# Performance work log

Hardware: AMD Instinct MI355X
Metric: run time of the kernel (lower is better)

## Reference

```python
import jax, jax.numpy as jnp
import numpy as np

H = 16
D_MODEL = 1024
D_K = D_MODEL // H
B, S = 4, 2048


def setup_inputs() -> dict:
    key = jax.random.key(0)
    ks = jax.random.split(key, 12)
    scale = 1.0 / np.sqrt(D_MODEL)
    inp = {
        "query": jax.random.normal(ks[0], (B, S, D_MODEL), jnp.float32),
        "key_in": jax.random.normal(ks[1], (B, S, D_MODEL), jnp.float32),
        "value": jax.random.normal(ks[2], (B, S, D_MODEL), jnp.float32),
        "mask": jax.random.randint(ks[3], (B, 1, S, S), 0, 2, jnp.int32),
    }
    # 4 Linear(d_model, d_model) layers: Wq, Wk, Wv, Wo (+ biases)
    names = ["q", "k", "v", "o"]
    for i, n in enumerate(names):
        inp[f"W{n}"] = jax.random.normal(ks[4 + i], (D_MODEL, D_MODEL), jnp.float32) * scale
        inp[f"b{n}"] = jax.random.normal(ks[8 + i], (D_MODEL,), jnp.float32) * scale
    return inp


def reference(query, key_in, value, mask, Wq, bq, Wk, bk, Wv, bv, Wo, bo):
    # Linear projections then split heads: [B,S,D] -> [B,H,S,Dk]
    def proj(x, W, b):
        y = jnp.einsum("bsd,ed->bse", x, W) + b  # torch Linear: x @ W.T + b
        return y.reshape(B, S, H, D_K).transpose(0, 2, 1, 3)

    q = proj(query, Wq, bq)
    k = proj(key_in, Wk, bk)
    v = proj(value, Wv, bv)

    scores = jnp.einsum("bhqd,bhkd->bhqk", q, k) / jnp.sqrt(jnp.float32(D_K))
    scores = jnp.where(mask == 0, jnp.float32(-1e9), scores)
    p_attn = jax.nn.softmax(scores, axis=-1)
    # dropout is identity in eval mode
    x = jnp.einsum("bhqk,bhkd->bhqd", p_attn, v)
    x = x.transpose(0, 2, 1, 3).reshape(B, S, D_MODEL)
    return jnp.einsum("bsd,ed->bse", x, Wo) + bo
```

## Files before the change

### kernel.cpp

```cpp
#include <hip/hip_runtime.h>
#include <hip/hip_bf16.h>

typedef __bf16 bf16_t;
typedef __attribute__((ext_vector_type(8))) __bf16 bf16x8;
typedef __attribute__((ext_vector_type(4))) __bf16 bf16x4;
typedef __attribute__((ext_vector_type(4))) float f32x4;
typedef __attribute__((ext_vector_type(16))) float f32x16;

#define GAS __attribute__((address_space(1)))
#define LAS __attribute__((address_space(3)))

__device__ __forceinline__ void async_copy16(const bf16_t* g, bf16_t* l) {
    __builtin_amdgcn_global_load_lds((const GAS void*)g, (LAS void*)l, 16, 0, 0);
}

__global__ __launch_bounds__(256) void convert_kernel(
    const float* __restrict__ src, bf16_t* __restrict__ dst, int n)
{
    int i = (blockIdx.x * 256 + threadIdx.x) * 8;
    if (i >= n) return;
    f32x4 f0 = *(const f32x4*)(src + i);
    f32x4 f1 = *(const f32x4*)(src + i + 4);
    bf16x8 v;
#pragma unroll
    for (int j = 0; j < 4; j++) { v[j] = (bf16_t)f0[j]; v[4 + j] = (bf16_t)f1[j]; }
    *(bf16x8*)&dst[i] = v;
}

__global__ __launch_bounds__(256) void pack_mask_kernel(
    const int* __restrict__ mask, unsigned long long* __restrict__ out)
{
    int i = blockIdx.x * 256 + threadIdx.x;
    unsigned long long bits = __ballot(mask[i] != 0);
    if ((threadIdx.x & 63) == 0) out[i >> 6] = bits;
}

template<int MODE>
__global__ __launch_bounds__(256, 2) void gemm_nt(
    const bf16_t* __restrict__ A, const bf16_t* __restrict__ W,
    const float* __restrict__ bias, void* __restrict__ out_, float oscale)
{
    __shared__ __align__(16) bf16_t Als[128 * 32];
    __shared__ __align__(16) bf16_t Bls[128 * 32];

    const int tid  = threadIdx.x;
    const int wave = tid >> 6, lane = tid & 63;
    const int quad = lane >> 4, lq = lane & 15;
    const int wm = wave >> 1, wn = wave & 1;
    const int tm = blockIdx.x * 128, tn = blockIdx.y * 128;
    const int K = 1024;

    const bf16_t* gA0 = A + (size_t)(tm + wave * 32 + (lane >> 2)) * K + (lane & 3) * 8;
    const bf16_t* gA1 = gA0 + (size_t)16 * K;
    const bf16_t* gB0 = W + (size_t)(tn + wave * 32 + (lane >> 2)) * K + (lane & 3) * 8;
    const bf16_t* gB1 = gB0 + (size_t)16 * K;
    bf16_t* lA0 = &Als[(wave * 32) * 32];
    bf16_t* lA1 = &Als[(wave * 32 + 16) * 32];
    bf16_t* lB0 = &Bls[(wave * 32) * 32];
    bf16_t* lB1 = &Bls[(wave * 32 + 16) * 32];

    f32x4 acc[4][4] = {};

    for (int k0 = 0; k0 < K; k0 += 32) {
        __syncthreads();
        async_copy16(gA0, lA0);
        async_copy16(gA1, lA1);
        async_copy16(gB0, lB0);
        async_copy16(gB1, lB1);
        gA0 += 32; gA1 += 32; gB0 += 32; gB1 += 32;
        __syncthreads();

        bf16x8 af[4], bfr[4];
#pragma unroll
        for (int i = 0; i < 4; i++) {
            af[i]  = *(const bf16x8*)&Als[(wm * 64 + i * 16 + lq) * 32 + quad * 8];
            bfr[i] = *(const bf16x8*)&Bls[(wn * 64 + i * 16 + lq) * 32 + quad * 8];
        }
#pragma unroll
        for (int i = 0; i < 4; i++)
#pragma unroll
            for (int j = 0; j < 4; j++) {
                if (MODE == 2)
                    acc[i][j] = __builtin_amdgcn_mfma_f32_16x16x32_bf16(bfr[j], af[i], acc[i][j], 0, 0, 0);
                else
                    acc[i][j] = __builtin_amdgcn_mfma_f32_16x16x32_bf16(af[i], bfr[j], acc[i][j], 0, 0, 0);
            }
    }

    float* outf = (float*)out_;
    bf16_t* outb = (bf16_t*)out_;
#pragma unroll
    for (int i = 0; i < 4; i++)
#pragma unroll
        for (int j = 0; j < 4; j++)
#pragma unroll
            for (int r = 0; r < 4; r++) {
                float v = acc[i][j][r];
                if (MODE == 0) {
                    int row = tm + wm * 64 + i * 16 + quad * 4 + r;
                    int col = tn + wn * 64 + j * 16 + lq;
                    outf[(size_t)row * 1024 + col] = (v + bias[col]) * oscale;
                } else if (MODE == 1) {
                    int row = tm + wm * 64 + i * 16 + quad * 4 + r;
                    int col = tn + wn * 64 + j * 16 + lq;
                    v = (v + bias[col]) * oscale;
                    int b = row >> 11, s = row & 2047;
                    int h = col >> 6,  dk = col & 63;
                    outb[(((size_t)(b * 16 + h) * 2048 + s) << 6) + dk] = (bf16_t)v;
                } else {
                    int n = tn + wn * 64 + j * 16 + quad * 4 + r;
                    int m = tm + wm * 64 + i * 16 + lq;
                    v = (v + bias[n]) * oscale;
                    int b = m >> 11, s = m & 2047;
                    int h = n >> 6,  dk = n & 63;
                    outb[((size_t)((b * 16 + h) * 64 + dk) << 11) + s] = (bf16_t)v;
                }
            }
}

#define LDP 68

__global__ __launch_bounds__(64, 2) void attn_kernel(
    const bf16_t* __restrict__ Q, const bf16_t* __restrict__ Kh,
    const bf16_t* __restrict__ Vt, const unsigned int* __restrict__ mp,
    bf16_t* __restrict__ X)
{
    __shared__ __align__(16) bf16_t Pls[64 * LDP];

    const int lane = threadIdx.x;
    const int l31  = lane & 31;
    const int hi8  = (lane >> 5) * 8, hi4 = (lane >> 5) * 4;
    const int bh = blockIdx.y;
    const int b  = bh >> 4, h = bh & 15;
    const int qb = blockIdx.x * 64;

    bf16x8 qf[2][4];
#pragma unroll
    for (int qg = 0; qg < 2; qg++) {
        const bf16_t* qp = Q + ((size_t)bh * 2048 + qb + qg * 32 + l31) * 64 + hi8;
#pragma unroll
        for (int c = 0; c < 4; c++) qf[qg][c] = *(const bf16x8*)(qp + c * 16);
    }

    f32x16 od[2][2] = {};
    float lsum[2] = {0.f, 0.f};

    const bf16_t* kbase = Kh + ((size_t)bh * 2048 + l31) * 64 + hi8;
    const bf16_t* vb0   = Vt + ((size_t)bh * 64 + l31) * 2048 + hi8;
    const bf16_t* vb1   = vb0 + (size_t)32 * 2048;

    const unsigned long long* mq0 =
        (const unsigned long long*)mp + ((size_t)(b << 11) + qb + l31) * 32;
    const unsigned long long* mq1 = mq0 + 32 * 32;

    bf16_t* pw = &Pls[0];

    for (int kt = 0; kt < 32; kt++) {
        unsigned long long mw[2] = { mq0[kt], mq1[kt] };
        const bf16_t* kk = kbase + (size_t)(kt * 64) * 64;

#pragma unroll
        for (int kh = 0; kh < 2; kh++) {
            bf16x8 kf[4];
            const bf16_t* krow = kk + (size_t)(kh * 32) * 64;
#pragma unroll
            for (int c = 0; c < 4; c++)
                kf[c] = *(const bf16x8*)(krow + c * 16);

#pragma unroll
            for (int qg = 0; qg < 2; qg++) {
                f32x16 z = {};
                z = __builtin_amdgcn_mfma_f32_32x32x16_bf16(kf[0], qf[qg][0], z, 0, 0, 0);
                z = __builtin_amdgcn_mfma_f32_32x32x16_bf16(kf[1], qf[qg][1], z, 0, 0, 0);
                z = __builtin_amdgcn_mfma_f32_32x32x16_bf16(kf[2], qf[qg][2], z, 0, 0, 0);
                z = __builtin_amdgcn_mfma_f32_32x32x16_bf16(kf[3], qf[qg][3], z, 0, 0, 0);
                unsigned int mbits = (unsigned int)(mw[qg] >> (kh * 32 + hi4));
                float ls = 0.f;
#pragma unroll
                for (int p = 0; p < 4; p++) {
                    bf16x4 pk;
#pragma unroll
                    for (int r = 0; r < 4; r++) {
                        float sv = ((mbits >> (8 * p + r)) & 1) ? z[4 * p + r] : -1e9f;
                        float e = __expf(sv);
                        ls += e;
                        pk[r] = (bf16_t)e;
                    }
                    *(bf16x4*)&pw[(qg * 32 + l31) * LDP + kh * 32 + 8 * p + hi4] = pk;
                }
                lsum[qg] += ls;
            }
        }

#pragma unroll
        for (int kh = 0; kh < 2; kh++) {
            bf16x8 pf[2][2];
#pragma unroll
            for (int qg = 0; qg < 2; qg++) {
                const bf16_t* prow = &pw[(qg * 32 + l31) * LDP + kh * 32 + hi8];
                pf[qg][0] = *(const bf16x8*)(prow);
                pf[qg][1] = *(const bf16x8*)(prow + 16);
            }
            const size_t voff = (size_t)(kt * 64 + kh * 32);
#pragma unroll
            for (int c = 0; c < 2; c++) {
                bf16x8 vf0 = *(const bf16x8*)(vb0 + voff + c * 16);
                bf16x8 vf1 = *(const bf16x8*)(vb1 + voff + c * 16);
                od[0][0] = __builtin_amdgcn_mfma_f32_32x32x16_bf16(vf0, pf[0][c], od[0][0], 0, 0, 0);
                od[1][0] = __builtin_amdgcn_mfma_f32_32x32x16_bf16(vf0, pf[1][c], od[1][0], 0, 0, 0);
                od[0][1] = __builtin_amdgcn_mfma_f32_32x32x16_bf16(vf1, pf[0][c], od[0][1], 0, 0, 0);
                od[1][1] = __builtin_amdgcn_mfma_f32_32x32x16_bf16(vf1, pf[1][c], od[1][1], 0, 0, 0);
            }
        }
    }

#pragma unroll
    for (int qg = 0; qg < 2; qg++) {
        float l = lsum[qg] + __shfl_xor(lsum[qg], 32);
        float rl = (l > 0.f) ? 1.0f / l : 0.f;
        int qrow = qb + qg * 32 + l31;
        bf16_t* xp = X + ((size_t)(b * 2048) + qrow) * 1024 + h * 64 + hi4;
#pragma unroll
        for (int dt = 0; dt < 2; dt++)
#pragma unroll
            for (int p = 0; p < 4; p++) {
                bf16x4 ov;
#pragma unroll
                for (int r = 0; r < 4; r++)
                    ov[r] = (bf16_t)(od[qg][dt][p * 4 + r] * rl);
                *(bf16x4*)(xp + dt * 32 + p * 8) = ov;
            }
    }
}

extern "C" void kernel_launch(void* const* d_in, const int* in_sizes, int n_in,
                              void* d_out, int out_size, void* d_ws, size_t ws_size,
                              hipStream_t stream)
{
    const float* query  = (const float*)d_in[0];
    const float* key_in = (const float*)d_in[1];
    const float* value  = (const float*)d_in[2];
    const int*   mask   = (const int*)d_in[3];

    char* ws = (char*)d_ws;
    const size_t SZ  = (size_t)8192 * 1024 * 2;
    const size_t MPK = (size_t)2 * 1024 * 1024;
    const size_t WSZ = (size_t)1024 * 1024 * 2;
    bf16_t* C   = (bf16_t*)(ws);
    bf16_t* Qb  = (bf16_t*)(ws + SZ);
    bf16_t* Kb  = (bf16_t*)(ws + 2 * SZ);
    bf16_t* Vtb = (bf16_t*)(ws + 3 * SZ);
    unsigned long long* mpack = (unsigned long long*)(ws + 4 * SZ);
    bf16_t* Wc[4];
    for (int i = 0; i < 4; i++)
        Wc[i] = (bf16_t*)(ws + 4 * SZ + MPK + i * WSZ);

    const size_t NEED = 4 * SZ + MPK + 4 * WSZ;
    if (ws_size < NEED) return;

    const int NACT = 8192 * 1024;
    for (int i = 0; i < 4; i++)
        convert_kernel<<<512, 256, 0, stream>>>((const float*)d_in[4 + 2 * i],
                                                Wc[i], 1024 * 1024);
    pack_mask_kernel<<<65536, 256, 0, stream>>>(mask, mpack);

    dim3 gg(64, 8);
    convert_kernel<<<4096, 256, 0, stream>>>(query, C, NACT);
    gemm_nt<1><<<gg, 256, 0, stream>>>(C, Wc[0], (const float*)d_in[5], Qb, 0.125f);
    convert_kernel<<<4096, 256, 0, stream>>>(key_in, C, NACT);
    gemm_nt<1><<<gg, 256, 0, stream>>>(C, Wc[1], (const float*)d_in[7], Kb, 1.0f);
    convert_kernel<<<4096, 256, 0, stream>>>(value, C, NACT);
    gemm_nt<2><<<gg, 256, 0, stream>>>(C, Wc[2], (const float*)d_in[9], Vtb, 1.0f);

    attn_kernel<<<dim3(32, 64), 64, 0, stream>>>(Qb, Kb, Vtb,
                                                 (const unsigned int*)mpack, C);
    gemm_nt<0><<<gg, 256, 0, stream>>>(C, Wc[3], (const float*)d_in[11], d_out, 1.0f);
}
```

Before: 486.6 us.

## Split attention key range across two waves with LDS reduction

The attention kernel now runs two waves per block, and each wave handles half of the 2048 keys (split-K) with its own LDS P buffer. At the end, wave 1 writes its partial output accumulators and row sums to LDS, and wave 0 adds them and writes the normalized result. The aim is to double the waves in flight per query tile and hide more latency. The cost is an extra LDS reduction, two barriers, more LDS per block, and a tighter register budget under launch_bounds(128,4). The softmax has no running max, so adding the two partial sums stays valid.

```diff
diff --git a/kernel.cpp b/kernel.cpp
--- a/kernel.cpp
+++ b/kernel.cpp
@@ -120,19 +120,21 @@
 
 #define LDP 68
 
-__global__ __launch_bounds__(64, 2) void attn_kernel(
+__global__ __launch_bounds__(128, 4) void attn_kernel(
     const bf16_t* __restrict__ Q, const bf16_t* __restrict__ Kh,
     const bf16_t* __restrict__ Vt, const unsigned int* __restrict__ mp,
     bf16_t* __restrict__ X)
 {
-    __shared__ __align__(16) bf16_t Pls[64 * LDP];
-
-    const int lane = threadIdx.x;
+    __shared__ __align__(16) bf16_t Pls[2][64 * LDP];
+
+    const int tid  = threadIdx.x;
+    const int wave = tid >> 6, lane = tid & 63;
     const int l31  = lane & 31;
     const int hi8  = (lane >> 5) * 8, hi4 = (lane >> 5) * 4;
     const int bh = blockIdx.y;
     const int b  = bh >> 4, h = bh & 15;
     const int qb = blockIdx.x * 64;
+    const int k0 = wave << 10;
 
     bf16x8 qf[2][4];
 #pragma unroll
@@ -145,17 +147,17 @@
     f32x16 od[2][2] = {};
     float lsum[2] = {0.f, 0.f};
 
-    const bf16_t* kbase = Kh + ((size_t)bh * 2048 + l31) * 64 + hi8;
-    const bf16_t* vb0   = Vt + ((size_t)bh * 64 + l31) * 2048 + hi8;
+    const bf16_t* kbase = Kh + ((size_t)bh * 2048 + k0 + l31) * 64 + hi8;
+    const bf16_t* vb0   = Vt + ((size_t)bh * 64 + l31) * 2048 + k0 + hi8;
     const bf16_t* vb1   = vb0 + (size_t)32 * 2048;
 
     const unsigned long long* mq0 =
-        (const unsigned long long*)mp + ((size_t)(b << 11) + qb + l31) * 32;
+        (const unsigned long long*)mp + ((size_t)(b << 11) + qb + l31) * 32 + wave * 16;
     const unsigned long long* mq1 = mq0 + 32 * 32;
 
-    bf16_t* pw = &Pls[0];
-
-    for (int kt = 0; kt < 32; kt++) {
+    bf16_t* pw = &Pls[wave][0];
+
+    for (int kt = 0; kt < 16; kt++) {
         unsigned long long mw[2] = { mq0[kt], mq1[kt] };
         const bf16_t* kk = kbase + (size_t)(kt * 64) * 64;
 
@@ -214,22 +216,55 @@
         }
     }
 
-#pragma unroll
-    for (int qg = 0; qg < 2; qg++) {
-        float l = lsum[qg] + __shfl_xor(lsum[qg], 32);
-        float rl = (l > 0.f) ? 1.0f / l : 0.f;
-        int qrow = qb + qg * 32 + l31;
-        bf16_t* xp = X + ((size_t)(b * 2048) + qrow) * 1024 + h * 64 + hi4;
-#pragma unroll
-        for (int dt = 0; dt < 2; dt++)
-#pragma unroll
-            for (int p = 0; p < 4; p++) {
-                bf16x4 ov;
-#pragma unroll
-                for (int r = 0; r < 4; r++)
-                    ov[r] = (bf16_t)(od[qg][dt][p * 4 + r] * rl);
-                *(bf16x4*)(xp + dt * 32 + p * 8) = ov;
-            }
+    float* cb = (float*)&Pls[0][0];
+    __syncthreads();
+    if (wave == 1) {
+        float* cl = cb + lane * 68;
+#pragma unroll
+        for (int qg = 0; qg < 2; qg++)
+#pragma unroll
+            for (int dt = 0; dt < 2; dt++)
+#pragma unroll
+                for (int p = 0; p < 4; p++) {
+                    f32x4 v4 = { od[qg][dt][4 * p], od[qg][dt][4 * p + 1],
+                                 od[qg][dt][4 * p + 2], od[qg][dt][4 * p + 3] };
+                    *(f32x4*)(cl + qg * 32 + dt * 16 + 4 * p) = v4;
+                }
+        cl[64] = lsum[0];
+        cl[65] = lsum[1];
+    }
+    __syncthreads();
+    if (wave == 0) {
+        const float* cl = cb + lane * 68;
+#pragma unroll
+        for (int qg = 0; qg < 2; qg++) {
+            lsum[qg] += cl[64 + qg];
+#pragma unroll
+            for (int dt = 0; dt < 2; dt++)
+#pragma unroll
+                for (int p = 0; p < 4; p++) {
+                    f32x4 v4 = *(const f32x4*)(cl + qg * 32 + dt * 16 + 4 * p);
+#pragma unroll
+                    for (int r = 0; r < 4; r++) od[qg][dt][4 * p + r] += v4[r];
+                }
+        }
+#pragma unroll
+        for (int qg = 0; qg < 2; qg++) {
+            float l = lsum[qg] + __shfl_xor(lsum[qg], 32);
+            float rl = (l > 0.f) ? 1.0f / l : 0.f;
+            int qrow = qb + qg * 32 + l31;
+            bf16_t* xp = X + ((size_t)(b * 2048) + qrow) * 1024 + h * 64 + hi4;
+#pragma unroll
+            for (int dt = 0; dt < 2; dt++)
+#pragma unroll
+                for (int p = 0; p < 4; p++) {
+                    bf16x4 ov;
+#pragma unroll
+                    for (int r = 0; r < 4; r++)
+                        ov[r] = (bf16_t)(od[qg][dt][p * 4 + r] * rl);
+                    *(bf16x4*)(xp + dt * 32 + p * 8) = ov;
+                }
+        }
     }
 }
 
@@ -272,7 +307,7 @@
     convert_kernel<<<4096, 256, 0, stream>>>(value, C, NACT);
     gemm_nt<2><<<gg, 256, 0, stream>>>(C, Wc[2], (const float*)d_in[9], Vtb, 1.0f);
 
-    attn_kernel<<<dim3(32, 64), 64, 0, stream>>>(Qb, Kb, Vtb,
-                                                 (const unsigned int*)mpack, C);
+    attn_kernel<<<dim3(32, 64), 128, 0, stream>>>(Qb, Kb, Vtb,
+                                                  (const unsigned int*)mpack, C);
     gemm_nt<0><<<gg, 256, 0, stream>>>(C, Wc[3], (const float*)d_in[11], d_out, 1.0f);
 }
```

Measured after the change: 784.5 us. +61.2%, slower.
